# Kernel tuning notes

Measured on AMD Instinct MI355X. Metric: run time of the kernel, lower is better.

Reference implementation:

```python
import jax, jax.numpy as jnp
import numpy as np

N_NODES = 50000
N_GRAPHS = 128
IN_DIM = 512
HID = 512
N_LAYERS = 3


def setup_inputs() -> dict:
    key = jax.random.key(0)
    ks = jax.random.split(key, 12)
    inp = {
        "x": jax.random.normal(ks[0], (N_NODES, IN_DIM), dtype=jnp.float32),
        "walk2": jax.random.randint(ks[1], (3, N_NODES), 0, N_NODES, dtype=jnp.int32),
        "walk3": jax.random.randint(ks[2], (4, N_NODES), 0, N_NODES, dtype=jnp.int32),
        "walk4": jax.random.randint(ks[3], (5, N_NODES), 0, N_NODES, dtype=jnp.int32),
        "batch": jnp.sort(jax.random.randint(ks[4], (N_NODES,), 0, N_GRAPHS, dtype=jnp.int32)),
    }
    dims = [IN_DIM, HID, HID]
    for i in range(N_LAYERS):
        scale = 1.0 / np.sqrt(dims[i])
        inp[f"W{i}"] = jax.random.normal(ks[5 + i], (dims[i], HID), dtype=jnp.float32) * scale
        inp[f"b{i}"] = jnp.zeros((HID,), dtype=jnp.float32)
    return inp


def _gather_sum(z, walk):
    # walk: [L, N] node indices -> sum of gathered embeddings, [N, H]
    L, N = walk.shape
    return jnp.take(z, walk.reshape(-1), axis=0).reshape(L, N, z.shape[1]).sum(0)


def reference(x, walk2, walk3, walk4, batch, W0, b0, W1, b1, W2, b2):
    layers = [(W0, b0), (W1, b1), (W2, b2)]
    path_batch = jnp.take(batch, walk2[0])  # [N]
    counts = jax.ops.segment_sum(jnp.ones((path_batch.shape[0],), jnp.float32),
                                 path_batch, num_segments=N_GRAPHS)
    denom = jnp.maximum(counts, 1.0)[:, None]  # avoid div-by-zero for empty graphs
    z = x
    g = []
    for W, b in layers:
        z = z @ W + b  # [N, H]
        path_emb = _gather_sum(z, walk2) + _gather_sum(z, walk3) + _gather_sum(z, walk4)
        pooled = jax.ops.segment_sum(path_emb, path_batch, num_segments=N_GRAPHS) / denom
        g.append(pooled)
    return jnp.concatenate(g, axis=1)  # [N_GRAPHS, 3*H]
```

## Files before the change

### kernel.cpp

```cpp
#include <hip/hip_runtime.h>

#define N_NODES 50000
#define N_GRAPHS 128
#define HID 512

#define KSPAN   256
#define KSPLIT  196
#define KPAD    (KSPAN * KSPLIT)
#define NPANEL  (KPAD / 16)

#define C8_OFF     0
#define C8_BYTES   ((size_t)N_GRAPHS * KPAD)
#define PSUM_OFF   (C8_OFF + C8_BYTES)
#define PSUM_BYTES ((size_t)N_GRAPHS * HID * 4)
#define COUNTS_OFF (PSUM_OFF + PSUM_BYTES)
#define ZERO_BYTES (COUNTS_OFF + 512)
#define APACK_OFF  ZERO_BYTES
#define APACK_BYTES ((size_t)NPANEL * 4 * 64 * 16)
#define PART_OFF   (APACK_OFF + APACK_BYTES)
#define PART_BYTES ((size_t)KSPLIT * N_GRAPHS * HID * 4)

typedef __attribute__((ext_vector_type(8))) short bf16x8;
typedef __attribute__((ext_vector_type(16))) float f32x16;

__global__ __launch_bounds__(256)
void build_c_kernel(const int* __restrict__ w2, const int* __restrict__ w3,
                    const int* __restrict__ w4, const int* __restrict__ batch,
                    unsigned int* __restrict__ C32, int* __restrict__ counts) {
    __shared__ int hist[N_GRAPHS];
    const int t = threadIdx.x;
    if (t < N_GRAPHS) hist[t] = 0;
    __syncthreads();
    const int i = blockIdx.x * 256 + t;
    if (i < N_NODES) {
        const int a = w2[i];
        const int g = batch[a];
        atomicAdd(&hist[g], 1);
        unsigned int* row = C32 + (size_t)g * (KPAD / 4);
        int nn[12];
        nn[0]  = a;
        nn[1]  = w2[N_NODES + i];
        nn[2]  = w2[2 * N_NODES + i];
        nn[3]  = w3[i];
        nn[4]  = w3[N_NODES + i];
        nn[5]  = w3[2 * N_NODES + i];
        nn[6]  = w3[3 * N_NODES + i];
        nn[7]  = w4[i];
        nn[8]  = w4[N_NODES + i];
        nn[9]  = w4[2 * N_NODES + i];
        nn[10] = w4[3 * N_NODES + i];
        nn[11] = w4[4 * N_NODES + i];
#pragma unroll
        for (int j = 0; j < 12; ++j) {
            const int nd = nn[j];
            atomicAdd(&row[nd >> 2], 1u << ((nd & 3) * 8));
        }
    }
    __syncthreads();
    if (t < N_GRAPHS) { const int hv = hist[t]; if (hv) atomicAdd(&counts[t], hv); }
}

__device__ inline unsigned pack_bf16(unsigned a, unsigned b) {
    return (__builtin_bit_cast(unsigned, (float)a) >> 16) |
           (__builtin_bit_cast(unsigned, (float)b) & 0xFFFF0000u);
}

__global__ __launch_bounds__(256)
void c8_to_apack_kernel(const unsigned char* __restrict__ C8,
                        uint4* __restrict__ Apack) {
    const int kp = blockIdx.x;
    const int t = threadIdx.x;
    const int mt = t >> 6;
    const int l = t & 63;
    const int row = mt * 32 + (l & 31);
    const int k0 = kp * 16 + 8 * (l >> 5);
    const uint2 b = *(const uint2*)(C8 + (size_t)row * KPAD + k0);
    uint4 o;
    o.x = pack_bf16(b.x & 0xFFu, (b.x >> 8) & 0xFFu);
    o.y = pack_bf16((b.x >> 16) & 0xFFu, b.x >> 24);
    o.z = pack_bf16(b.y & 0xFFu, (b.y >> 8) & 0xFFu);
    o.w = pack_bf16((b.y >> 16) & 0xFFu, b.y >> 24);
    Apack[(size_t)(kp * 4 + mt) * 64 + l] = o;
}

__device__ inline unsigned bpack(unsigned u0, unsigned u1) {
    return __builtin_amdgcn_perm(u1, u0, 0x07060302u);
}

__device__ inline f32x16 mfma_bf16(bf16x8 a, bf16x8 b, f32x16 c) {
    return __builtin_amdgcn_mfma_f32_32x32x16_bf16(a, b, c, 0, 0, 0);
}

template <int GUARD>
__device__ inline void issue_b7(const float* __restrict__ xp, int krow,
                                unsigned (&u)[8]) {
#pragma unroll
    for (int j = 0; j < 8; ++j) {
        int k = krow + j;
        if (GUARD) k = min(k, N_NODES - 1);
        u[j] = __builtin_bit_cast(unsigned, xp[(size_t)k * HID]);
    }
}

template <int GUARD>
__device__ inline void run_k7(const float* __restrict__ xp,
                              const uint4* __restrict__ ldsA,
                              int kbase, int h, int lane,
                              f32x16 (&acc)[4]) {
    unsigned bu[2][8];
    issue_b7<GUARD>(xp, kbase + 8 * h, bu[0]);
    issue_b7<GUARD>(xp, kbase + 16 + 8 * h, bu[1]);
#pragma unroll
    for (int s = 0; s < KSPAN / 16; ++s) {
        const int slot = s & 1;
        uint4 a[4];
#pragma unroll
        for (int mt = 0; mt < 4; ++mt)
            a[mt] = ldsA[(s * 4 + mt) * 64 + lane];
        unsigned d[4];
#pragma unroll
        for (int jj = 0; jj < 4; ++jj)
            d[jj] = bpack(bu[slot][2 * jj], bu[slot][2 * jj + 1]);
        const bf16x8 B = __builtin_bit_cast(bf16x8, make_uint4(d[0], d[1], d[2], d[3]));
        if (s + 2 < KSPAN / 16)
            issue_b7<GUARD>(xp, kbase + (s + 2) * 16 + 8 * h, bu[slot]);
#pragma unroll
        for (int mt = 0; mt < 4; ++mt)
            acc[mt] = mfma_bf16(__builtin_bit_cast(bf16x8, a[mt]), B, acc[mt]);
    }
}

template <int ATOMIC>
__global__ __launch_bounds__(512, 4)
void pool_gemm7_kernel(const float* __restrict__ x,
                       const uint4* __restrict__ Apack,
                       float* __restrict__ dst) {
    __shared__ uint4 ldsA[(KSPAN / 16) * 4 * 64];
    const int t = threadIdx.x;
    const int lane = t & 63;
    const int w = t >> 6;
    const int n = lane & 31;
    const int h = lane >> 5;
    const int chalf = blockIdx.x;
    const int ks = blockIdx.y;
    const int kbase = ks * KSPAN;
    const int kp0 = ks * (KSPAN / 16);

    {
        const uint4* src = Apack + (size_t)kp0 * 4 * 64;
#pragma unroll
        for (int i = 0; i < 8; ++i)
            ldsA[t + i * 512] = src[t + i * 512];
    }
    __syncthreads();

    f32x16 acc[4];
#pragma unroll
    for (int mt = 0; mt < 4; ++mt)
#pragma unroll
        for (int r = 0; r < 16; ++r) acc[mt][r] = 0.f;

    const int col = chalf * 256 + w * 32 + n;
    const float* xp = x + col;

    if (kbase + KSPAN <= N_NODES) run_k7<0>(xp, ldsA, kbase, h, lane, acc);
    else                          run_k7<1>(xp, ldsA, kbase, h, lane, acc);

    float* outp = ATOMIC ? dst : dst + (size_t)ks * (N_GRAPHS * HID);
#pragma unroll
    for (int mt = 0; mt < 4; ++mt)
#pragma unroll
        for (int i = 0; i < 16; ++i) {
            const int row = mt * 32 + (i & 3) + 8 * (i >> 2) + 4 * h;
            if (ATOMIC) atomicAdd(&outp[(size_t)row * HID + col], acc[mt][i]);
            else        outp[(size_t)row * HID + col] = acc[mt][i];
        }
}

__global__ __launch_bounds__(256)
void reduce_part_kernel(const float* __restrict__ part, float* __restrict__ Psum) {
    const int id = blockIdx.x * 256 + threadIdx.x;
    float s0 = 0.f, s1 = 0.f;
    for (int k = 0; k + 2 <= KSPLIT; k += 2) {
        s0 += part[(size_t)k * (N_GRAPHS * HID) + id];
        s1 += part[(size_t)(k + 1) * (N_GRAPHS * HID) + id];
    }
    Psum[id] = s0 + s1;
}

__global__ __launch_bounds__(256)
void layer_gemm_kernel(const float* __restrict__ A, int lda, int scaleA,
                       const float* __restrict__ W,
                       const float* __restrict__ bias,
                       const int* __restrict__ counts,
                       float* __restrict__ out) {
    __shared__ float Alds[16][128];
    const int ct = blockIdx.x, rt = blockIdx.y, ksb = blockIdx.z;
    const int t = threadIdx.x;
    const int cc = ct * 64 + (t & 63);
    const int wv = t >> 6;
    const int k0 = ksb * 128;

    for (int idx = t; idx < 16 * 32; idx += 256) {
        const int rr = idx >> 5;
        const int kk = (idx & 31) * 4;
        const int row = rt * 16 + rr;
        float4 v = *(const float4*)&A[(size_t)row * lda + k0 + kk];
        if (scaleA) {
            const float inv = 1.f / (float)max(counts[row], 1);
            v.x *= inv; v.y *= inv; v.z *= inv; v.w *= inv;
        }
        *(float4*)&Alds[rr][kk] = v;
    }
    __syncthreads();

    const int r0 = rt * 16 + wv * 4;
    float a0 = 0.f, a1 = 0.f, a2 = 0.f, a3 = 0.f;
#pragma unroll 8
    for (int k = 0; k < 128; ++k) {
        const float wval = W[(size_t)(k0 + k) * HID + cc];
        a0 += Alds[wv * 4 + 0][k] * wval;
        a1 += Alds[wv * 4 + 1][k] * wval;
        a2 += Alds[wv * 4 + 2][k] * wval;
        a3 += Alds[wv * 4 + 3][k] * wval;
    }
    if (ksb == 0) {
        const float bc = bias[cc];
        a0 += (counts[r0 + 0] > 0 ? 12.f : 0.f) * bc;
        a1 += (counts[r0 + 1] > 0 ? 12.f : 0.f) * bc;
        a2 += (counts[r0 + 2] > 0 ? 12.f : 0.f) * bc;
        a3 += (counts[r0 + 3] > 0 ? 12.f : 0.f) * bc;
    }
    atomicAdd(&out[(size_t)(r0 + 0) * 1536 + cc], a0);
    atomicAdd(&out[(size_t)(r0 + 1) * 1536 + cc], a1);
    atomicAdd(&out[(size_t)(r0 + 2) * 1536 + cc], a2);
    atomicAdd(&out[(size_t)(r0 + 3) * 1536 + cc], a3);
}

extern "C" void kernel_launch(void* const* d_in, const int* in_sizes, int n_in,
                              void* d_out, int out_size, void* d_ws, size_t ws_size,
                              hipStream_t stream) {
    const float* x     = (const float*)d_in[0];
    const int*   w2    = (const int*)d_in[1];
    const int*   w3    = (const int*)d_in[2];
    const int*   w4    = (const int*)d_in[3];
    const int*   batch = (const int*)d_in[4];
    const float* W0    = (const float*)d_in[5];
    const float* b0    = (const float*)d_in[6];
    const float* W1    = (const float*)d_in[7];
    const float* b1    = (const float*)d_in[8];
    const float* W2    = (const float*)d_in[9];
    const float* b2    = (const float*)d_in[10];
    float* out = (float*)d_out;

    unsigned char* ws  = (unsigned char*)d_ws;
    unsigned int* C32  = (unsigned int*)(ws + C8_OFF);
    float* Psum        = (float*)(ws + PSUM_OFF);
    int* counts        = (int*)(ws + COUNTS_OFF);
    uint4* Apack       = (uint4*)(ws + APACK_OFF);
    float* part        = (float*)(ws + PART_OFF);
    const bool use_part = ws_size >= PART_OFF + PART_BYTES;

    hipMemsetAsync(d_ws, 0, ZERO_BYTES, stream);
    hipMemsetAsync(d_out, 0, (size_t)out_size * 4, stream);

    build_c_kernel<<<(N_NODES + 255) / 256, 256, 0, stream>>>(w2, w3, w4, batch, C32, counts);
    c8_to_apack_kernel<<<NPANEL, 256, 0, stream>>>((const unsigned char*)C32, Apack);

    if (use_part) {
        pool_gemm7_kernel<0><<<dim3(2, KSPLIT), 512, 0, stream>>>(x, Apack, part);
        reduce_part_kernel<<<256, 256, 0, stream>>>(part, Psum);
    } else {
        pool_gemm7_kernel<1><<<dim3(2, KSPLIT), 512, 0, stream>>>(x, Apack, Psum);
    }

    layer_gemm_kernel<<<dim3(8, 8, 4), 256, 0, stream>>>(Psum, HID, 1, W0, b0, counts, out);
    layer_gemm_kernel<<<dim3(8, 8, 4), 256, 0, stream>>>(out, 1536, 0, W1, b1, counts, out + 512);
    layer_gemm_kernel<<<dim3(8, 8, 4), 256, 0, stream>>>(out + 512, 1536, 0, W2, b2, counts, out + 1024);
}
```

Baseline: 287.8 us.

## Use 1024-thread pool GEMM blocks covering all columns and split partial reduction

The pooling GEMM now launches one 1024-thread block per K-slice covering all 512 columns instead of two 512-thread blocks. The A panel is staged into LDS once per slice rather than twice. K span shrinks to 208 (13 steps) with 241 slices. The partial-sum reduction is split across four K ranges per output with atomic accumulation, raising parallelism at the cost of more partial-buffer traffic and atomics.

Result: faster. 271.9 us (-5.5%).

```diff
diff --git a/kernel.cpp b/kernel.cpp
--- a/kernel.cpp
+++ b/kernel.cpp
@@ -4,8 +4,8 @@
 #define N_GRAPHS 128
 #define HID 512
 
-#define KSPAN   256
-#define KSPLIT  196
+#define KSPAN   208
+#define KSPLIT  241
 #define KPAD    (KSPAN * KSPLIT)
 #define NPANEL  (KPAD / 16)
 
@@ -92,8 +92,8 @@
 }
 
 template <int GUARD>
-__device__ inline void issue_b7(const float* __restrict__ xp, int krow,
-                                unsigned (&u)[8]) {
+__device__ inline void issue_b(const float* __restrict__ xp, int krow,
+                               unsigned (&u)[8]) {
 #pragma unroll
     for (int j = 0; j < 8; ++j) {
         int k = krow + j;
@@ -103,15 +103,15 @@
 }
 
 template <int GUARD>
-__device__ inline void run_k7(const float* __restrict__ xp,
+__device__ inline void run_k8(const float* __restrict__ xp,
                               const uint4* __restrict__ ldsA,
                               int kbase, int h, int lane,
                               f32x16 (&acc)[4]) {
     unsigned bu[2][8];
-    issue_b7<GUARD>(xp, kbase + 8 * h, bu[0]);
-    issue_b7<GUARD>(xp, kbase + 16 + 8 * h, bu[1]);
-#pragma unroll
-    for (int s = 0; s < KSPAN / 16; ++s) {
+    issue_b<GUARD>(xp, kbase + 8 * h, bu[0]);
+    issue_b<GUARD>(xp, kbase + 16 + 8 * h, bu[1]);
+#pragma unroll
+    for (int s = 0; s < 13; ++s) {
         const int slot = s & 1;
         uint4 a[4];
 #pragma unroll
@@ -122,8 +122,8 @@
         for (int jj = 0; jj < 4; ++jj)
             d[jj] = bpack(bu[slot][2 * jj], bu[slot][2 * jj + 1]);
         const bf16x8 B = __builtin_bit_cast(bf16x8, make_uint4(d[0], d[1], d[2], d[3]));
-        if (s + 2 < KSPAN / 16)
-            issue_b7<GUARD>(xp, kbase + (s + 2) * 16 + 8 * h, bu[slot]);
+        if (s + 2 < 13)
+            issue_b<GUARD>(xp, kbase + (s + 2) * 16 + 8 * h, bu[slot]);
 #pragma unroll
         for (int mt = 0; mt < 4; ++mt)
             acc[mt] = mfma_bf16(__builtin_bit_cast(bf16x8, a[mt]), B, acc[mt]);
@@ -131,26 +131,23 @@
 }
 
 template <int ATOMIC>
-__global__ __launch_bounds__(512, 4)
-void pool_gemm7_kernel(const float* __restrict__ x,
+__global__ __launch_bounds__(1024, 4)
+void pool_gemm8_kernel(const float* __restrict__ x,
                        const uint4* __restrict__ Apack,
                        float* __restrict__ dst) {
-    __shared__ uint4 ldsA[(KSPAN / 16) * 4 * 64];
+    __shared__ uint4 ldsA[13 * 4 * 64];
     const int t = threadIdx.x;
     const int lane = t & 63;
     const int w = t >> 6;
     const int n = lane & 31;
     const int h = lane >> 5;
-    const int chalf = blockIdx.x;
-    const int ks = blockIdx.y;
+    const int ks = blockIdx.x;
     const int kbase = ks * KSPAN;
-    const int kp0 = ks * (KSPAN / 16);
 
     {
-        const uint4* src = Apack + (size_t)kp0 * 4 * 64;
-#pragma unroll
-        for (int i = 0; i < 8; ++i)
-            ldsA[t + i * 512] = src[t + i * 512];
+        const uint4* src = Apack + (size_t)(ks * 13) * 4 * 64;
+        for (int i = t; i < 13 * 4 * 64; i += 1024)
+            ldsA[i] = src[i];
     }
     __syncthreads();
 
@@ -160,11 +157,11 @@
 #pragma unroll
         for (int r = 0; r < 16; ++r) acc[mt][r] = 0.f;
 
-    const int col = chalf * 256 + w * 32 + n;
+    const int col = w * 32 + n;
     const float* xp = x + col;
 
-    if (kbase + KSPAN <= N_NODES) run_k7<0>(xp, ldsA, kbase, h, lane, acc);
-    else                          run_k7<1>(xp, ldsA, kbase, h, lane, acc);
+    if (kbase + KSPAN <= N_NODES) run_k8<0>(xp, ldsA, kbase, h, lane, acc);
+    else                          run_k8<1>(xp, ldsA, kbase, h, lane, acc);
 
     float* outp = ATOMIC ? dst : dst + (size_t)ks * (N_GRAPHS * HID);
 #pragma unroll
@@ -180,12 +177,18 @@
 __global__ __launch_bounds__(256)
 void reduce_part_kernel(const float* __restrict__ part, float* __restrict__ Psum) {
     const int id = blockIdx.x * 256 + threadIdx.x;
-    float s0 = 0.f, s1 = 0.f;
-    for (int k = 0; k + 2 <= KSPLIT; k += 2) {
+    const int kstart = blockIdx.y * 61;
+    const int kend = min(KSPLIT, kstart + 61);
+    float s0 = 0.f, s1 = 0.f, s2 = 0.f, s3 = 0.f;
+    int k = kstart;
+    for (; k + 4 <= kend; k += 4) {
         s0 += part[(size_t)k * (N_GRAPHS * HID) + id];
         s1 += part[(size_t)(k + 1) * (N_GRAPHS * HID) + id];
-    }
-    Psum[id] = s0 + s1;
+        s2 += part[(size_t)(k + 2) * (N_GRAPHS * HID) + id];
+        s3 += part[(size_t)(k + 3) * (N_GRAPHS * HID) + id];
+    }
+    for (; k < kend; ++k) s0 += part[(size_t)k * (N_GRAPHS * HID) + id];
+    atomicAdd(&Psum[id], (s0 + s1) + (s2 + s3));
 }
 
 __global__ __launch_bounds__(256)
@@ -268,10 +271,10 @@
     c8_to_apack_kernel<<<NPANEL, 256, 0, stream>>>((const unsigned char*)C32, Apack);
 
     if (use_part) {
-        pool_gemm7_kernel<0><<<dim3(2, KSPLIT), 512, 0, stream>>>(x, Apack, part);
-        reduce_part_kernel<<<256, 256, 0, stream>>>(part, Psum);
+        pool_gemm8_kernel<0><<<KSPLIT, 1024, 0, stream>>>(x, Apack, part);
+        reduce_part_kernel<<<dim3(256, 4), 256, 0, stream>>>(part, Psum);
     } else {
-        pool_gemm7_kernel<1><<<dim3(2, KSPLIT), 512, 0, stream>>>(x, Apack, Psum);
+        pool_gemm8_kernel<1><<<KSPLIT, 1024, 0, stream>>>(x, Apack, Psum);
     }
 
     layer_gemm_kernel<<<dim3(8, 8, 4), 256, 0, stream>>>(Psum, HID, 1, W0, b0, counts, out);
```
